# Kernel tuning notes

Measured on AMD Instinct MI355X. Metric: run time of the kernel, lower is better.

## Reference

```python
import jax, jax.numpy as jnp
import numpy as np

CODEBOOK_SIZE = 512
LATENT_DIM = 12
BATCH = 512
TOKENS = 256


def setup_inputs() -> dict:
    key = jax.random.key(0)
    k1, k2 = jax.random.split(key)
    x = jax.random.normal(k1, (BATCH, TOKENS, LATENT_DIM), dtype=jnp.float32)
    # nn.Embedding init: uniform(-1/K, 1/K)
    lim = 1.0 / CODEBOOK_SIZE
    codebook = jax.random.uniform(k2, (CODEBOOK_SIZE, LATENT_DIM), dtype=jnp.float32,
                                  minval=-lim, maxval=lim)
    return {"x": x, "codebook": codebook}


def reference(x, codebook):
    # same as for torch.cdist (sqrt is monotonic).
    x2 = jnp.sum(x * x, axis=-1, keepdims=True)            # [B, N, 1]
    w2 = jnp.sum(codebook * codebook, axis=-1)             # [K]
    xw = jnp.einsum('bnd,kd->bnk', x, codebook)            # [B, N, K]
    dist2 = x2 - 2.0 * xw + w2                             # [B, N, K]
    indices = jnp.argmin(dist2, axis=-1)                   # [B, N] int
    quantized = codebook[indices]                          # [B, N, D]

    codebook_loss = jnp.mean((quantized - jax.lax.stop_gradient(x)) ** 2)
    commitment_loss = 0.25 * jnp.mean((jax.lax.stop_gradient(quantized) - x) ** 2)
    quantize_loss = codebook_loss + commitment_loss

    # straight-through estimator
    quantized_st = x + jax.lax.stop_gradient(quantized - x)
    return quantized_st, indices, quantize_loss
```

## Files before the change

### kernel.cpp

```cpp
#include <hip/hip_runtime.h>
#include <math.h>

namespace {
constexpr int KCB   = 512;
constexpr int DIM   = 12;
constexpr int NTOK  = 512 * 256;
constexpr int QSIZE = NTOK * DIM;
constexpr int NSPLIT = 8;
constexpr int KCHUNK = KCB / NSPLIT;
constexpr int TPT    = 4;
constexpr int TOKS_PER_BLOCK = 64 * TPT;
constexpr int NBLK   = NTOK / TOKS_PER_BLOCK;
constexpr int WVEC_FLOATS = KCB * DIM;
constexpr int CB_FLOATS   = WVEC_FLOATS + KCB;
constexpr int CB_F4       = CB_FLOATS / 4;
constexpr int SMEM_U64    = 3328;

__global__ __launch_bounds__(256) void pack_cb(const float* __restrict__ cb,
                                               float* __restrict__ ws,
                                               float* __restrict__ out) {
    int k = blockIdx.x * blockDim.x + threadIdx.x;
    if (k == 0) out[QSIZE + NTOK] = 0.f;
    if (k >= KCB) return;
    float w[DIM];
#pragma unroll
    for (int d = 0; d < DIM; ++d) w[d] = cb[k * DIM + d];
    float w2 = 0.f;
#pragma unroll
    for (int d = 0; d < DIM; ++d) w2 += w[d] * w[d];
#pragma unroll
    for (int d = 0; d < DIM; ++d) ws[k * DIM + d] = w[d];
    ws[WVEC_FLOATS + k] = w2;
}

__device__ inline float code_score(const float (&xv)[DIM], float x2,
                                   const float4& c0, const float4& c1,
                                   const float4& c2, float w2k) {
    float xw = 0.f;
    xw = fmaf(xv[0],  c0.x, xw);
    xw = fmaf(xv[1],  c0.y, xw);
    xw = fmaf(xv[2],  c0.z, xw);
    xw = fmaf(xv[3],  c0.w, xw);
    xw = fmaf(xv[4],  c1.x, xw);
    xw = fmaf(xv[5],  c1.y, xw);
    xw = fmaf(xv[6],  c1.z, xw);
    xw = fmaf(xv[7],  c1.w, xw);
    xw = fmaf(xv[8],  c2.x, xw);
    xw = fmaf(xv[9],  c2.y, xw);
    xw = fmaf(xv[10], c2.z, xw);
    xw = fmaf(xv[11], c2.w, xw);
    return fmaf(-2.f, xw, x2) + w2k;
}

__global__ __launch_bounds__(512, 2) void vq_main(const float* __restrict__ x,
                                                  const float* __restrict__ cb,
                                                  const float* __restrict__ pk,
                                                  float* __restrict__ out) {
    __shared__ unsigned long long smem[SMEM_U64];
    float* lds = (float*)smem;
    const int tid  = threadIdx.x;
    const int lane = tid & 63;
    const int s = __builtin_amdgcn_readfirstlane(tid >> 6);
    const int tbase = blockIdx.x * TOKS_PER_BLOCK;

    {
        float4* l4 = (float4*)lds;
        const float4* g4 = (const float4*)pk;
        for (int i = tid; i < CB_F4; i += 512) l4[i] = g4[i];
    }

    float xs[TPT][DIM];
    float x2[TPT];
#pragma unroll
    for (int j = 0; j < TPT; ++j) {
        const float4* xp = (const float4*)(x + (size_t)(tbase + j * 64 + lane) * DIM);
        float4 a0 = xp[0], a1 = xp[1], a2 = xp[2];
        xs[j][0] = a0.x; xs[j][1] = a0.y; xs[j][2]  = a0.z; xs[j][3]  = a0.w;
        xs[j][4] = a1.x; xs[j][5] = a1.y; xs[j][6]  = a1.z; xs[j][7]  = a1.w;
        xs[j][8] = a2.x; xs[j][9] = a2.y; xs[j][10] = a2.z; xs[j][11] = a2.w;
        float t2 = 0.f;
#pragma unroll
        for (int d = 0; d < DIM; ++d) t2 = fmaf(xs[j][d], xs[j][d], t2);
        x2[j] = t2;
    }

    __syncthreads();

    float best[TPT];
    int   bi[TPT];
#pragma unroll
    for (int j = 0; j < TPT; ++j) { best[j] = INFINITY; bi[j] = 0; }

    const int k0 = s * KCHUNK;
    const float* w2v = lds + WVEC_FLOATS;
#pragma unroll 2
    for (int g = 0; g < KCHUNK / 4; ++g) {
        float4 w2q = ((const float4*)w2v)[(k0 >> 2) + g];
        const float* cbase = lds + (size_t)(k0 + 4 * g) * DIM;
#pragma unroll
        for (int u = 0; u < 4; ++u) {
            float4 c0 = *(const float4*)(cbase + u * DIM + 0);
            float4 c1 = *(const float4*)(cbase + u * DIM + 4);
            float4 c2 = *(const float4*)(cbase + u * DIM + 8);
            float w2k = (u == 0) ? w2q.x : (u == 1) ? w2q.y : (u == 2) ? w2q.z : w2q.w;
            const int k = k0 + 4 * g + u;
#pragma unroll
            for (int j = 0; j < TPT; ++j) {
                float d = code_score(xs[j], x2[j], c0, c1, c2, w2k);
                bool c = d < best[j];
                best[j] = c ? d : best[j];
                bi[j]   = c ? k : bi[j];
            }
        }
    }

    auto mkkey = [](float v, int k) {
        unsigned su = __float_as_uint(v);
        su = (su & 0x80000000u) ? ~su : (su | 0x80000000u);
        return ((unsigned long long)su << 32) | (unsigned)k;
    };
    __syncthreads();
#pragma unroll
    for (int j = 0; j < TPT; ++j)
        smem[s * TOKS_PER_BLOCK + j * 64 + lane] = mkkey(best[j], bi[j]);
    __syncthreads();

    if (s < TPT) {
        const int tok = s * 64 + lane;
        unsigned long long m = smem[tok];
#pragma unroll
        for (int r = 1; r < NSPLIT; ++r) {
            unsigned long long v = smem[r * TOKS_PER_BLOCK + tok];
            m = v < m ? v : m;
        }
        const int bid = (int)(m & 0xffffffffULL);
        unsigned eu = (unsigned)(m >> 32);
        unsigned orig = (eu & 0x80000000u) ? (eu ^ 0x80000000u) : ~eu;
        const float bsc = __uint_as_float(orig);
        const int t = tbase + tok;

        float xv[DIM];
#pragma unroll
        for (int j = 0; j < TPT; ++j)
            if (j == s) {
#pragma unroll
                for (int d = 0; d < DIM; ++d) xv[d] = xs[j][d];
            }

        const float4* wrow = (const float4*)(cb + (size_t)bid * DIM);
        float4 q0 = wrow[0], q1 = wrow[1], q2 = wrow[2];
        float qs[DIM] = {q0.x, q0.y, q0.z, q0.w, q1.x, q1.y, q1.z, q1.w,
                         q2.x, q2.y, q2.z, q2.w};

        float4* qo = (float4*)(out + (size_t)t * DIM);
        float4 r0, r1, r2;
        r0.x = xv[0] + (qs[0] - xv[0]);    r0.y = xv[1] + (qs[1] - xv[1]);
        r0.z = xv[2] + (qs[2] - xv[2]);    r0.w = xv[3] + (qs[3] - xv[3]);
        r1.x = xv[4] + (qs[4] - xv[4]);    r1.y = xv[5] + (qs[5] - xv[5]);
        r1.z = xv[6] + (qs[6] - xv[6]);    r1.w = xv[7] + (qs[7] - xv[7]);
        r2.x = xv[8] + (qs[8] - xv[8]);    r2.y = xv[9] + (qs[9] - xv[9]);
        r2.z = xv[10] + (qs[10] - xv[10]); r2.w = xv[11] + (qs[11] - xv[11]);
        qo[0] = r0; qo[1] = r1; qo[2] = r2;

        out[QSIZE + t] = (float)bid;

        float ls = bsc * (1.25f / (float)QSIZE);
#pragma unroll
        for (int off = 32; off > 0; off >>= 1) ls += __shfl_down(ls, off);
        if (lane == 0) atomicAdd(out + QSIZE + NTOK, ls);
    }
}
}

extern "C" void kernel_launch(void* const* d_in, const int* in_sizes, int n_in,
                              void* d_out, int out_size, void* d_ws, size_t ws_size,
                              hipStream_t stream) {
    const float* x  = (const float*)d_in[0];
    const float* cb = (const float*)d_in[1];
    float* out = (float*)d_out;
    float* pk  = (float*)d_ws;

    pack_cb<<<2, 256, 0, stream>>>(cb, pk, out);
    vq_main<<<NBLK, 512, 0, stream>>>(x, cb, pk, out);
}
```

Measured before the change: 107.7 us.

## Software-pipeline codebook LDS loads and replace loss atomics with deterministic two-stage reduction

The distance loop now double-buffers codebook rows in registers, loading the next code while scoring the current one, so LDS latency overlaps with FMA work. The global atomicAdd for the loss is replaced by per-block partial sums written to workspace and a third kernel that reduces the 512 partials. This removes contended atomics and makes the sum deterministic, at the cost of an extra kernel launch and a few more registers.

```diff
diff --git a/kernel.cpp b/kernel.cpp
--- a/kernel.cpp
+++ b/kernel.cpp
@@ -14,13 +14,12 @@
 constexpr int WVEC_FLOATS = KCB * DIM;
 constexpr int CB_FLOATS   = WVEC_FLOATS + KCB;
 constexpr int CB_F4       = CB_FLOATS / 4;
-constexpr int SMEM_U64    = 3328;
+constexpr int SMEM_U64    = 3333;
+constexpr int PARTIALS_OFF = 8192;
 
 __global__ __launch_bounds__(256) void pack_cb(const float* __restrict__ cb,
-                                               float* __restrict__ ws,
-                                               float* __restrict__ out) {
+                                               float* __restrict__ ws) {
     int k = blockIdx.x * blockDim.x + threadIdx.x;
-    if (k == 0) out[QSIZE + NTOK] = 0.f;
     if (k >= KCB) return;
     float w[DIM];
 #pragma unroll
@@ -55,8 +54,10 @@
 __global__ __launch_bounds__(512, 2) void vq_main(const float* __restrict__ x,
                                                   const float* __restrict__ cb,
                                                   const float* __restrict__ pk,
-                                                  float* __restrict__ out) {
+                                                  float* __restrict__ out,
+                                                  float* __restrict__ partials) {
     __shared__ unsigned long long smem[SMEM_U64];
+    __shared__ float lred[TPT];
     float* lds = (float*)smem;
     const int tid  = threadIdx.x;
     const int lane = tid & 63;
@@ -93,20 +94,47 @@
 
     const int k0 = s * KCHUNK;
     const float* w2v = lds + WVEC_FLOATS;
-#pragma unroll 2
-    for (int g = 0; g < KCHUNK / 4; ++g) {
-        float4 w2q = ((const float4*)w2v)[(k0 >> 2) + g];
-        const float* cbase = lds + (size_t)(k0 + 4 * g) * DIM;
-#pragma unroll
-        for (int u = 0; u < 4; ++u) {
-            float4 c0 = *(const float4*)(cbase + u * DIM + 0);
-            float4 c1 = *(const float4*)(cbase + u * DIM + 4);
-            float4 c2 = *(const float4*)(cbase + u * DIM + 8);
-            float w2k = (u == 0) ? w2q.x : (u == 1) ? w2q.y : (u == 2) ? w2q.z : w2q.w;
-            const int k = k0 + 4 * g + u;
+
+    float4 A0, A1, A2; float w2A;
+    float4 B0, B1, B2; float w2B;
+    {
+        const float* c = lds + (size_t)k0 * DIM;
+        A0 = *(const float4*)(c + 0);
+        A1 = *(const float4*)(c + 4);
+        A2 = *(const float4*)(c + 8);
+        w2A = w2v[k0];
+    }
+#pragma unroll 4
+    for (int kk = 0; kk < KCHUNK; kk += 2) {
+        {
+            const float* c = lds + (size_t)(k0 + kk + 1) * DIM;
+            B0 = *(const float4*)(c + 0);
+            B1 = *(const float4*)(c + 4);
+            B2 = *(const float4*)(c + 8);
+            w2B = w2v[k0 + kk + 1];
+        }
+        {
+            const int k = k0 + kk;
 #pragma unroll
             for (int j = 0; j < TPT; ++j) {
-                float d = code_score(xs[j], x2[j], c0, c1, c2, w2k);
+                float d = code_score(xs[j], x2[j], A0, A1, A2, w2A);
+                bool c = d < best[j];
+                best[j] = c ? d : best[j];
+                bi[j]   = c ? k : bi[j];
+            }
+        }
+        {
+            const float* c = lds + (size_t)(k0 + kk + 2) * DIM;
+            A0 = *(const float4*)(c + 0);
+            A1 = *(const float4*)(c + 4);
+            A2 = *(const float4*)(c + 8);
+            w2A = w2v[k0 + kk + 2];
+        }
+        {
+            const int k = k0 + kk + 1;
+#pragma unroll
+            for (int j = 0; j < TPT; ++j) {
+                float d = code_score(xs[j], x2[j], B0, B1, B2, w2B);
                 bool c = d < best[j];
                 best[j] = c ? d : best[j];
                 bi[j]   = c ? k : bi[j];
@@ -167,7 +195,26 @@
         float ls = bsc * (1.25f / (float)QSIZE);
 #pragma unroll
         for (int off = 32; off > 0; off >>= 1) ls += __shfl_down(ls, off);
-        if (lane == 0) atomicAdd(out + QSIZE + NTOK, ls);
+        if (lane == 0) lred[s] = ls;
+    }
+    __syncthreads();
+    if (tid == 0)
+        partials[blockIdx.x] = (lred[0] + lred[1]) + (lred[2] + lred[3]);
+}
+
+__global__ __launch_bounds__(512) void reduce_loss(const float* __restrict__ partials,
+                                                   float* __restrict__ out) {
+    __shared__ float r[8];
+    float v = partials[threadIdx.x];
+#pragma unroll
+    for (int off = 32; off > 0; off >>= 1) v += __shfl_down(v, off);
+    if ((threadIdx.x & 63) == 0) r[threadIdx.x >> 6] = v;
+    __syncthreads();
+    if (threadIdx.x == 0) {
+        float t = 0.f;
+#pragma unroll
+        for (int i = 0; i < 8; ++i) t += r[i];
+        out[QSIZE + NTOK] = t;
     }
 }
 }
@@ -179,7 +226,9 @@
     const float* cb = (const float*)d_in[1];
     float* out = (float*)d_out;
     float* pk  = (float*)d_ws;
-
-    pack_cb<<<2, 256, 0, stream>>>(cb, pk, out);
-    vq_main<<<NBLK, 512, 0, stream>>>(x, cb, pk, out);
-}
+    float* partials = (float*)d_ws + PARTIALS_OFF;
+
+    pack_cb<<<2, 256, 0, stream>>>(cb, pk);
+    vq_main<<<NBLK, 512, 0, stream>>>(x, cb, pk, out, partials);
+    reduce_loss<<<1, 512, 0, stream>>>(partials, out);
+}
```

Result: faster. 93.89 us (-12.8%).
